# Optimization experiments

Hardware: AMD Instinct MI355X
Metric: run time of the kernel (lower is better)

Reference implementation:

```python
import jax, jax.numpy as jnp
import numpy as np

N_HEADS = 8
HEAD_DIM = 64
SCALE = HEAD_DIM ** -0.5


def setup_inputs() -> dict:
    key = jax.random.key(0)
    k1, k2, k3 = jax.random.split(key, 3)
    B, C, Hs, Ws = 8, 512, 64, 64
    x = jax.random.normal(k1, (B, C, Hs, Ws), dtype=jnp.float32)
    _h = jnp.zeros((1,), dtype=jnp.int32)  # unused arg in original forward
    # proj_in: Linear(C, 3*H*hd); stored as (in, out) so y = x @ W + b
    W_in = jax.random.normal(k2, (C, 3 * N_HEADS * HEAD_DIM), dtype=jnp.float32) * (C ** -0.5)
    b_in = jnp.zeros((3 * N_HEADS * HEAD_DIM,), dtype=jnp.float32)
    W_out = jax.random.normal(k3, (N_HEADS * HEAD_DIM, C), dtype=jnp.float32) * ((N_HEADS * HEAD_DIM) ** -0.5)
    b_out = jnp.zeros((C,), dtype=jnp.float32)
    return {"x": x, "_h": _h, "W_in": W_in, "b_in": b_in, "W_out": W_out, "b_out": b_out}


def reference(x, _h, W_in, b_in, W_out, b_out):
    in_shape = x.shape
    B, C = in_shape[0], in_shape[1]
    # (B, C, *spatial) -> (B, S, C)
    xf = x.reshape(B, C, -1).transpose(0, 2, 1)
    S = xf.shape[1]
    # fused QKV projection -> (B, S, H, 3*hd), chunk into q, k, v: (B, S, H, hd)
    qkv = (xf @ W_in + b_in).reshape(B, S, N_HEADS, 3 * HEAD_DIM)
    q, k, v = jnp.split(qkv, 3, axis=-1)
    # NOTE: faithful to the original, SDPA receives (B, S, H, hd) WITHOUT a
    # transpose to (B, H, S, hd): attention runs over the heads axis (HxH),
    # batched over (B, S).
    scores = jnp.einsum("bsqd,bskd->bsqk", q, k) * SCALE  # (B, S, H, H)
    attn = jax.nn.softmax(scores, axis=-1)
    out = jnp.einsum("bsqk,bskd->bsqd", attn, v)  # (B, S, H, hd)
    out = out.reshape(B, S, N_HEADS * HEAD_DIM)
    out = out @ W_out + b_out  # (B, S, C)
    return out.transpose(0, 2, 1).reshape(in_shape)
```

## Files before the change

### kernel.cpp

```cpp
#include <hip/hip_runtime.h>
#include <hip/hip_bf16.h>

typedef __attribute__((ext_vector_type(8))) short bh8;
typedef __attribute__((ext_vector_type(4))) float fx4;

#define GLOAD16(g, l)                                                          \
  __builtin_amdgcn_global_load_lds(                                            \
      (const __attribute__((address_space(1))) void*)(g),                      \
      (__attribute__((address_space(3))) void*)(l), 16, 0, 0)

__device__ __forceinline__ unsigned short f2bf(float f) {
  unsigned int u = __float_as_uint(f);
  u += 0x7fffu + ((u >> 16) & 1u);
  return (unsigned short)(u >> 16);
}
__device__ __forceinline__ float bf2f(short h) {
  return __uint_as_float(((unsigned int)(unsigned short)h) << 16);
}

__global__ __launch_bounds__(256) void transpose_cvt(
    const float* __restrict__ in, short* __restrict__ out, int R, int Ccols) {
  __shared__ float tile[64][65];
  const int b = blockIdx.z;
  const int c0 = blockIdx.x * 64;
  const int r0 = blockIdx.y * 64;
  const float* ip = in + (size_t)b * R * Ccols;
  short* op = out + (size_t)b * Ccols * R;
  const int tid = threadIdx.x;
  const int tx = tid & 63, ty = tid >> 6;
#pragma unroll
  for (int i = 0; i < 16; ++i) {
    int r = ty + i * 4;
    tile[tx][r] = ip[(size_t)(r0 + r) * Ccols + c0 + tx];
  }
  __syncthreads();
  const int cg = tid & 15;
  const int rr = tid >> 4;
#pragma unroll
  for (int i = 0; i < 4; ++i) {
    const int cc = i * 16 + rr;
    const unsigned int lo = (unsigned int)f2bf(tile[cc][cg * 4 + 0]) |
                            ((unsigned int)f2bf(tile[cc][cg * 4 + 1]) << 16);
    const unsigned int hi = (unsigned int)f2bf(tile[cc][cg * 4 + 2]) |
                            ((unsigned int)f2bf(tile[cc][cg * 4 + 3]) << 16);
    uint2 v; v.x = lo; v.y = hi;
    *(uint2*)&op[(size_t)(c0 + cc) * R + r0 + cg * 4] = v;
  }
}

template <int MODE, int KC>
__global__ __launch_bounds__(256) void gemm_bt(
    const short* __restrict__ A, const short* __restrict__ Bt,
    const float* __restrict__ bias, void* __restrict__ Cout,
    int M, int N, int tok0) {
  __shared__ short As[3][128 * 32] __attribute__((aligned(16)));
  __shared__ short Bs[3][128 * 32] __attribute__((aligned(16)));
  constexpr int NT = KC / 32;
  const int tid = threadIdx.x;
  const int lane = tid & 63;
  const int wv = tid >> 6;
  const int wr = wv >> 1, wc = wv & 1;

  const int nbx = gridDim.x, nby = gridDim.y;
  const int nwg = nbx * nby;
  int h = blockIdx.y * nbx + blockIdx.x;
  int L = h;
  if ((nwg & 7) == 0) {
    const int q = nwg >> 3;
    L = (h & 7) * q + (h >> 3);
  }
  int bx, by;
  if (MODE == 1) {
    by = L / nbx;
    bx = L - by * nbx;
  } else {
    bx = L / nby;
    by = L - bx * nby;
  }
  const int m0 = by * 128, n0 = bx * 128;

  const int lr = lane & 15;
  const int lk = (lane >> 4) * 8;
  const int rsw = ((lr >> 1) & 3) << 3;

  fx4 acc[4][4] = {};

  const int srow = tid >> 2;
  const int skoff = (((tid & 3) ^ ((tid >> 3) & 3)) * 8);
  const size_t abase = (size_t)(m0 + srow) * KC + skoff;
  const size_t bbase = (size_t)(n0 + srow) * KC + skoff;
  const int ldoff = wv * 1024;

  auto STAGE = [&](int kt, int slot) {
    const size_t ko = (size_t)kt * 32;
    char* lA = (char*)As[slot] + ldoff;
    char* lB = (char*)Bs[slot] + ldoff;
    GLOAD16(A + abase + ko, lA);
    GLOAD16(A + abase + (size_t)64 * KC + ko, lA + 4096);
    GLOAD16(Bt + bbase + ko, lB);
    GLOAD16(Bt + bbase + (size_t)64 * KC + ko, lB + 4096);
  };

  STAGE(0, 0);
  STAGE(1, 1);

  for (int t = 0; t < NT; ++t) {
    __builtin_amdgcn_sched_barrier(0);
    if (t < NT - 1) {
      asm volatile("s_waitcnt vmcnt(4)" ::: "memory");
    } else {
      asm volatile("s_waitcnt vmcnt(0)" ::: "memory");
    }
    __builtin_amdgcn_s_barrier();
    __builtin_amdgcn_sched_barrier(0);
    if (t + 2 < NT) STAGE(t + 2, (t + 2) % 3);
    __builtin_amdgcn_sched_barrier(0);

    const int sl = t % 3;
    bh8 af[4], bfm[4];
#pragma unroll
    for (int i = 0; i < 4; ++i) {
      af[i] = *(const bh8*)&As[sl][(wr * 64 + i * 16 + lr) * 32 + (lk ^ rsw)];
      bfm[i] = *(const bh8*)&Bs[sl][(wc * 64 + i * 16 + lr) * 32 + (lk ^ rsw)];
    }
#pragma unroll
    for (int i = 0; i < 4; ++i)
#pragma unroll
      for (int j = 0; j < 4; ++j)
        acc[i][j] = __builtin_amdgcn_mfma_f32_16x16x32_bf16(af[i], bfm[j],
                                                            acc[i][j], 0, 0, 0);
  }

  if (MODE == 1) {
    short* C = (short*)Cout;
#pragma unroll
    for (int i = 0; i < 4; ++i) {
      const int gm = m0 + wr * 64 + i * 16 + (lane >> 4) * 4;
#pragma unroll
      for (int j = 0; j < 4; ++j) {
        const int gn = n0 + wc * 64 + j * 16 + lr;
        const float bv = bias[gn];
#pragma unroll
        for (int r = 0; r < 4; ++r)
          C[(size_t)(gm + r) * N + gn] = (short)f2bf(acc[i][j][r] + bv);
      }
    }
  } else {
    float* C = (float*)Cout;
#pragma unroll
    for (int i = 0; i < 4; ++i) {
      const int ch0 = m0 + wr * 64 + i * 16 + (lane >> 4) * 4;
#pragma unroll
      for (int j = 0; j < 4; ++j) {
        const int t = tok0 + n0 + wc * 64 + j * 16 + lr;
        const int bb = t >> 12, s = t & 4095;
#pragma unroll
        for (int r = 0; r < 4; ++r) {
          const int ch = ch0 + r;
          C[((size_t)(bb * 512 + ch)) * 4096 + s] = acc[i][j][r] + bias[ch];
        }
      }
    }
  }
}

__global__ __launch_bounds__(256) void attn_kernel(
    const short* __restrict__ QKV, short* __restrict__ AO) {
  __shared__ short sq[4][1536] __attribute__((aligned(16)));
  const int tid = threadIdx.x, lane = tid & 63, wv = tid >> 6;
  const int t = blockIdx.x * 4 + wv;

  {
    const short* g = QKV + (size_t)t * 1536 + lane * 8;
    char* l = (char*)&sq[wv][0];
    GLOAD16(g, l);
    GLOAD16(g + 512, l + 1024);
    GLOAD16(g + 1024, l + 2048);
  }
  asm volatile("s_waitcnt vmcnt(0)" ::: "memory");

  const int i = lane >> 3, j = lane & 7;
  const short* q = &sq[wv][i * 192];
  const short* k = &sq[wv][j * 192 + 64];
  float s = 0.f;
#pragma unroll
  for (int c = 0; c < 8; ++c) {
    bh8 qa = *(const bh8*)&q[c * 8];
    bh8 ka = *(const bh8*)&k[c * 8];
#pragma unroll
    for (int e = 0; e < 8; ++e) s += bf2f(qa[e]) * bf2f(ka[e]);
  }
  s *= 0.125f;

  float m = s;
  m = fmaxf(m, __shfl_xor(m, 1));
  m = fmaxf(m, __shfl_xor(m, 2));
  m = fmaxf(m, __shfl_xor(m, 4));
  float p = __expf(s - m);
  float sum = p;
  sum += __shfl_xor(sum, 1);
  sum += __shfl_xor(sum, 2);
  sum += __shfl_xor(sum, 4);
  const float a = p / sum;

  float o[8] = {};
#pragma unroll
  for (int jj = 0; jj < 8; ++jj) {
    const float aj = __shfl(a, (lane & 56) | jj);
    bh8 va = *(const bh8*)&sq[wv][jj * 192 + 128 + j * 8];
#pragma unroll
    for (int e = 0; e < 8; ++e) o[e] += aj * bf2f(va[e]);
  }
  bh8 ov;
#pragma unroll
  for (int e = 0; e < 8; ++e) ov[e] = (short)f2bf(o[e]);
  *(bh8*)&AO[(size_t)t * 512 + i * 64 + j * 8] = ov;
}

extern "C" void kernel_launch(void* const* d_in, const int* in_sizes, int n_in,
                              void* d_out, int out_size, void* d_ws,
                              size_t ws_size, hipStream_t stream) {
  const float* x = (const float*)d_in[0];
  const float* W_in = (const float*)d_in[2];
  const float* b_in = (const float*)d_in[3];
  const float* W_out = (const float*)d_in[4];
  const float* b_out = (const float*)d_in[5];
  float* out = (float*)d_out;

  short* Xbf = (short*)d_ws;
  short* WinT = Xbf + (size_t)32768 * 512;
  short* WoutT = WinT + (size_t)1536 * 512;
  short* QKVc = WoutT + (size_t)512 * 512;

  const size_t fixed_bytes =
      ((size_t)32768 * 512 + (size_t)1536 * 512 + (size_t)512 * 512) * 2;
  int NC = 1;
  while (NC < 256 &&
         fixed_bytes + ((size_t)32768 / NC) * 1536 * 2 > ws_size)
    NC <<= 1;
  const int Mc = 32768 / NC;

  transpose_cvt<<<dim3(64, 8, 8), 256, 0, stream>>>(x, Xbf, 512, 4096);
  transpose_cvt<<<dim3(24, 8, 1), 256, 0, stream>>>(W_in, WinT, 512, 1536);
  transpose_cvt<<<dim3(8, 8, 1), 256, 0, stream>>>(W_out, WoutT, 512, 512);

  for (int c = 0; c < NC; ++c) {
    const int t0 = c * Mc;
    short* Ach = Xbf + (size_t)t0 * 512;
    gemm_bt<1, 512><<<dim3(12, Mc / 128), 256, 0, stream>>>(Ach, WinT, b_in,
                                                            QKVc, Mc, 1536, 0);
    attn_kernel<<<dim3(Mc / 4), 256, 0, stream>>>(QKVc, Ach);
    gemm_bt<2, 512><<<dim3(Mc / 128, 4), 256, 0, stream>>>(WoutT, Ach, b_out,
                                                           out, 512, Mc, t0);
  }
}
```

Baseline: 243.7 us.

## Enlarge GEMM tiles to 256x256 with 8 waves and split-stage double buffering

The bf16 GEMM kernel moves from 128x128 tiles with 4 waves and a 3-slot LDS ring to 256x256 tiles with 8 waves (2x4 wave grid, 128x64 per wave) and a double buffer. Each k-step is split into two halves: the loads for one operand are issued first and the loads for the other are issued mid-step, with s_setprio raised around the MFMA bursts. The goal is more data reuse per global load and better overlap of loads with compute. In exchange it uses more accumulator registers and launches fewer, larger blocks, which could lower occupancy or leave some CUs idle on the small grids.

```diff
diff --git a/kernel.cpp b/kernel.cpp
--- a/kernel.cpp
+++ b/kernel.cpp
@@ -49,17 +49,18 @@
 }
 
 template <int MODE, int KC>
-__global__ __launch_bounds__(256) void gemm_bt(
+__global__ __launch_bounds__(512, 2) void gemm_bt(
     const short* __restrict__ A, const short* __restrict__ Bt,
     const float* __restrict__ bias, void* __restrict__ Cout,
     int M, int N, int tok0) {
-  __shared__ short As[3][128 * 32] __attribute__((aligned(16)));
-  __shared__ short Bs[3][128 * 32] __attribute__((aligned(16)));
+  __shared__ short As[2][8192] __attribute__((aligned(16)));
+  __shared__ short Bs[2][8192] __attribute__((aligned(16)));
   constexpr int NT = KC / 32;
   const int tid = threadIdx.x;
   const int lane = tid & 63;
   const int wv = tid >> 6;
-  const int wr = wv >> 1, wc = wv & 1;
+  const int wm = wv >> 2;
+  const int wn = wv & 3;
 
   const int nbx = gridDim.x, nby = gridDim.y;
   const int nwg = nbx * nby;
@@ -69,76 +70,106 @@
     const int q = nwg >> 3;
     L = (h & 7) * q + (h >> 3);
   }
-  int bx, by;
-  if (MODE == 1) {
-    by = L / nbx;
-    bx = L - by * nbx;
-  } else {
-    bx = L / nby;
-    by = L - bx * nby;
-  }
-  const int m0 = by * 128, n0 = bx * 128;
+  const int bx = L / nby;
+  const int by = L - bx * nby;
+  const int m0 = by * 256, n0 = bx * 256;
 
   const int lr = lane & 15;
-  const int lk = (lane >> 4) * 8;
-  const int rsw = ((lr >> 1) & 3) << 3;
-
-  fx4 acc[4][4] = {};
+  const int kg = lane >> 4;
+  const int rsw = (kg ^ ((lr >> 1) & 3)) * 8;
 
   const int srow = tid >> 2;
-  const int skoff = (((tid & 3) ^ ((tid >> 3) & 3)) * 8);
-  const size_t abase = (size_t)(m0 + srow) * KC + skoff;
-  const size_t bbase = (size_t)(n0 + srow) * KC + skoff;
-  const int ldoff = wv * 1024;
-
-  auto STAGE = [&](int kt, int slot) {
-    const size_t ko = (size_t)kt * 32;
-    char* lA = (char*)As[slot] + ldoff;
-    char* lB = (char*)Bs[slot] + ldoff;
-    GLOAD16(A + abase + ko, lA);
-    GLOAD16(A + abase + (size_t)64 * KC + ko, lA + 4096);
-    GLOAD16(Bt + bbase + ko, lB);
-    GLOAD16(Bt + bbase + (size_t)64 * KC + ko, lB + 4096);
-  };
-
-  STAGE(0, 0);
-  STAGE(1, 1);
-
-  for (int t = 0; t < NT; ++t) {
+  const int schunk = ((tid & 3) ^ ((tid >> 3) & 3)) * 8;
+  const size_t abase = (size_t)(m0 + srow) * KC + schunk;
+  const size_t bbase = (size_t)(n0 + srow) * KC + schunk;
+  const int doff = tid * 16;
+
+#define SA(kt, b, hh)                                                          \
+  GLOAD16(A + abase + (size_t)(hh)*128 * KC + (kt)*32,                         \
+          (char*)&As[b][0] + (hh)*8192 + doff)
+#define SB(kt, b, hh)                                                          \
+  GLOAD16(Bt + bbase + (size_t)(hh)*128 * KC + (kt)*32,                        \
+          (char*)&Bs[b][0] + (hh)*8192 + doff)
+
+  fx4 acc[8][4] = {};
+
+  SA(0, 0, 0); SA(0, 0, 1); SB(0, 0, 0); SB(0, 0, 1);
+
+#define MF16(a0_, a1_, a2_, a3_, r0_)                                          \
+  {                                                                            \
+    _Pragma("unroll") for (int j = 0; j < 4; ++j) {                            \
+      acc[r0_ + 0][j] =                                                        \
+          __builtin_amdgcn_mfma_f32_16x16x32_bf16(a0_, bb[j], acc[r0_ + 0][j], 0, 0, 0); \
+      acc[r0_ + 1][j] =                                                        \
+          __builtin_amdgcn_mfma_f32_16x16x32_bf16(a1_, bb[j], acc[r0_ + 1][j], 0, 0, 0); \
+      acc[r0_ + 2][j] =                                                        \
+          __builtin_amdgcn_mfma_f32_16x16x32_bf16(a2_, bb[j], acc[r0_ + 2][j], 0, 0, 0); \
+      acc[r0_ + 3][j] =                                                        \
+          __builtin_amdgcn_mfma_f32_16x16x32_bf16(a3_, bb[j], acc[r0_ + 3][j], 0, 0, 0); \
+    }                                                                          \
+  }
+
+  for (int g = 0; g < NT; ++g) {
+    const int buf = g & 1, nb = buf ^ 1;
+    const short* Ab = &As[buf][0];
+    const short* Bb = &Bs[buf][0];
+
     __builtin_amdgcn_sched_barrier(0);
-    if (t < NT - 1) {
-      asm volatile("s_waitcnt vmcnt(4)" ::: "memory");
+    if (g + 1 < NT) {
+      if (MODE == 1) { SA(g + 1, nb, 0); SA(g + 1, nb, 1); }
+      else           { SB(g + 1, nb, 0); SB(g + 1, nb, 1); }
+      __builtin_amdgcn_sched_barrier(0);
+      asm volatile("s_waitcnt vmcnt(2)" ::: "memory");
     } else {
       asm volatile("s_waitcnt vmcnt(0)" ::: "memory");
     }
     __builtin_amdgcn_s_barrier();
     __builtin_amdgcn_sched_barrier(0);
-    if (t + 2 < NT) STAGE(t + 2, (t + 2) % 3);
-    __builtin_amdgcn_sched_barrier(0);
-
-    const int sl = t % 3;
-    bh8 af[4], bfm[4];
-#pragma unroll
-    for (int i = 0; i < 4; ++i) {
-      af[i] = *(const bh8*)&As[sl][(wr * 64 + i * 16 + lr) * 32 + (lk ^ rsw)];
-      bfm[i] = *(const bh8*)&Bs[sl][(wc * 64 + i * 16 + lr) * 32 + (lk ^ rsw)];
-    }
-#pragma unroll
-    for (int i = 0; i < 4; ++i)
+    {
+      bh8 a0 = *(const bh8*)&Ab[(wm * 128 + 0 + lr) * 32 + rsw];
+      bh8 a1 = *(const bh8*)&Ab[(wm * 128 + 16 + lr) * 32 + rsw];
+      bh8 a2 = *(const bh8*)&Ab[(wm * 128 + 32 + lr) * 32 + rsw];
+      bh8 a3 = *(const bh8*)&Ab[(wm * 128 + 48 + lr) * 32 + rsw];
+      bh8 bb[4];
 #pragma unroll
       for (int j = 0; j < 4; ++j)
-        acc[i][j] = __builtin_amdgcn_mfma_f32_16x16x32_bf16(af[i], bfm[j],
-                                                            acc[i][j], 0, 0, 0);
+        bb[j] = *(const bh8*)&Bb[(wn * 64 + j * 16 + lr) * 32 + rsw];
+      asm volatile("s_waitcnt lgkmcnt(0)" ::: "memory");
+      __builtin_amdgcn_sched_barrier(0);
+      __builtin_amdgcn_s_setprio(1);
+      MF16(a0, a1, a2, a3, 0);
+      __builtin_amdgcn_s_setprio(0);
+      __builtin_amdgcn_sched_barrier(0);
+      __builtin_amdgcn_s_barrier();
+
+      a0 = *(const bh8*)&Ab[(wm * 128 + 64 + 0 + lr) * 32 + rsw];
+      a1 = *(const bh8*)&Ab[(wm * 128 + 64 + 16 + lr) * 32 + rsw];
+      a2 = *(const bh8*)&Ab[(wm * 128 + 64 + 32 + lr) * 32 + rsw];
+      a3 = *(const bh8*)&Ab[(wm * 128 + 64 + 48 + lr) * 32 + rsw];
+      if (g + 1 < NT) {
+        if (MODE == 1) { SB(g + 1, nb, 0); SB(g + 1, nb, 1); }
+        else           { SA(g + 1, nb, 0); SA(g + 1, nb, 1); }
+      }
+      __builtin_amdgcn_sched_barrier(0);
+      __builtin_amdgcn_s_barrier();
+      asm volatile("s_waitcnt lgkmcnt(0)" ::: "memory");
+      __builtin_amdgcn_sched_barrier(0);
+      __builtin_amdgcn_s_setprio(1);
+      MF16(a0, a1, a2, a3, 4);
+      __builtin_amdgcn_s_setprio(0);
+      __builtin_amdgcn_sched_barrier(0);
+      __builtin_amdgcn_s_barrier();
+    }
   }
 
   if (MODE == 1) {
     short* C = (short*)Cout;
 #pragma unroll
-    for (int i = 0; i < 4; ++i) {
-      const int gm = m0 + wr * 64 + i * 16 + (lane >> 4) * 4;
+    for (int i = 0; i < 8; ++i) {
+      const int gm = m0 + wm * 128 + i * 16 + kg * 4;
 #pragma unroll
       for (int j = 0; j < 4; ++j) {
-        const int gn = n0 + wc * 64 + j * 16 + lr;
+        const int gn = n0 + wn * 64 + j * 16 + lr;
         const float bv = bias[gn];
 #pragma unroll
         for (int r = 0; r < 4; ++r)
@@ -148,20 +179,23 @@
   } else {
     float* C = (float*)Cout;
 #pragma unroll
-    for (int i = 0; i < 4; ++i) {
-      const int ch0 = m0 + wr * 64 + i * 16 + (lane >> 4) * 4;
+    for (int i = 0; i < 8; ++i) {
+      const int ch0 = m0 + wm * 128 + i * 16 + kg * 4;
 #pragma unroll
       for (int j = 0; j < 4; ++j) {
-        const int t = tok0 + n0 + wc * 64 + j * 16 + lr;
-        const int bb = t >> 12, s = t & 4095;
+        const int t = tok0 + n0 + wn * 64 + j * 16 + lr;
+        const int bb2 = t >> 12, s = t & 4095;
 #pragma unroll
         for (int r = 0; r < 4; ++r) {
           const int ch = ch0 + r;
-          C[((size_t)(bb * 512 + ch)) * 4096 + s] = acc[i][j][r] + bias[ch];
+          C[((size_t)(bb2 * 512 + ch)) * 4096 + s] = acc[i][j][r] + bias[ch];
         }
       }
     }
   }
+#undef SA
+#undef SB
+#undef MF16
 }
 
 __global__ __launch_bounds__(256) void attn_kernel(
@@ -235,7 +269,7 @@
   const size_t fixed_bytes =
       ((size_t)32768 * 512 + (size_t)1536 * 512 + (size_t)512 * 512) * 2;
   int NC = 1;
-  while (NC < 256 &&
+  while (NC < 128 &&
          fixed_bytes + ((size_t)32768 / NC) * 1536 * 2 > ws_size)
     NC <<= 1;
   const int Mc = 32768 / NC;
@@ -247,10 +281,10 @@
   for (int c = 0; c < NC; ++c) {
     const int t0 = c * Mc;
     short* Ach = Xbf + (size_t)t0 * 512;
-    gemm_bt<1, 512><<<dim3(12, Mc / 128), 256, 0, stream>>>(Ach, WinT, b_in,
-                                                            QKVc, Mc, 1536, 0);
+    gemm_bt<1, 512><<<dim3(6, Mc / 256), 512, 0, stream>>>(Ach, WinT, b_in,
+                                                           QKVc, Mc, 1536, 0);
     attn_kernel<<<dim3(Mc / 4), 256, 0, stream>>>(QKVc, Ach);
-    gemm_bt<2, 512><<<dim3(Mc / 128, 4), 256, 0, stream>>>(WoutT, Ach, b_out,
+    gemm_bt<2, 512><<<dim3(Mc / 256, 2), 512, 0, stream>>>(WoutT, Ach, b_out,
                                                            out, 512, Mc, t0);
   }
 }
```

Result: slower. 258.4 us (+6.0%).

## Enlarge GEMM tiles to 256x128 with 8 waves and 64-wide K stages

Applied to the files above, without the earlier changes.

Both GEMMs now use 512-thread blocks computing 256x128 output tiles with K staged in 64-element chunks. A is triple-buffered and B double-buffered, with a new 8-chunk XOR swizzle in LDS. The goal is to reuse each B tile across twice as many rows and to halve the number of barriers per K. In exchange each block uses more LDS (about 128 KB) and occupancy drops to one block per CU, and the grids get smaller. The chunk-count cap is also lowered.

```diff
diff --git a/kernel.cpp b/kernel.cpp
--- a/kernel.cpp
+++ b/kernel.cpp
@@ -49,17 +49,18 @@
 }
 
 template <int MODE, int KC>
-__global__ __launch_bounds__(256) void gemm_bt(
+__global__ __launch_bounds__(512, 1) void gemm_bt(
     const short* __restrict__ A, const short* __restrict__ Bt,
     const float* __restrict__ bias, void* __restrict__ Cout,
     int M, int N, int tok0) {
-  __shared__ short As[3][128 * 32] __attribute__((aligned(16)));
-  __shared__ short Bs[3][128 * 32] __attribute__((aligned(16)));
-  constexpr int NT = KC / 32;
+  __shared__ short As[3][256 * 64] __attribute__((aligned(16)));
+  __shared__ short Bs[2][128 * 64] __attribute__((aligned(16)));
+  constexpr int NS = KC / 64;
   const int tid = threadIdx.x;
   const int lane = tid & 63;
   const int wv = tid >> 6;
-  const int wr = wv >> 1, wc = wv & 1;
+  const int wm = wv >> 1;
+  const int wn = wv & 1;
 
   const int nbx = gridDim.x, nby = gridDim.y;
   const int nwg = nbx * nby;
@@ -77,68 +78,80 @@
     bx = L / nby;
     by = L - bx * nby;
   }
-  const int m0 = by * 128, n0 = bx * 128;
+  const int m0 = by * 256, n0 = bx * 128;
 
   const int lr = lane & 15;
-  const int lk = (lane >> 4) * 8;
-  const int rsw = ((lr >> 1) & 3) << 3;
+  const int kg = lane >> 4;
+
+  const int schunk = ((tid & 7) ^ ((tid >> 3) & 7)) * 8;
+  const size_t abase = (size_t)(m0 + (tid >> 3)) * KC + schunk;
+  const size_t bbase = (size_t)(n0 + (tid >> 3)) * KC + schunk;
+
+  auto STAGE_A = [&](int s) {
+    const int buf = s % 3;
+    const size_t ko = (size_t)s * 64;
+#pragma unroll
+    for (int q = 0; q < 4; ++q)
+      GLOAD16(A + abase + (size_t)q * 64 * KC + ko,
+              (char*)&As[buf][0] + q * 8192 + tid * 16);
+  };
+  auto STAGE_B = [&](int s) {
+    const int buf = s & 1;
+    const size_t ko = (size_t)s * 64;
+#pragma unroll
+    for (int q = 0; q < 2; ++q)
+      GLOAD16(Bt + bbase + (size_t)q * 64 * KC + ko,
+              (char*)&Bs[buf][0] + q * 8192 + tid * 16);
+  };
 
   fx4 acc[4][4] = {};
 
-  const int srow = tid >> 2;
-  const int skoff = (((tid & 3) ^ ((tid >> 3) & 3)) * 8);
-  const size_t abase = (size_t)(m0 + srow) * KC + skoff;
-  const size_t bbase = (size_t)(n0 + srow) * KC + skoff;
-  const int ldoff = wv * 1024;
-
-  auto STAGE = [&](int kt, int slot) {
-    const size_t ko = (size_t)kt * 32;
-    char* lA = (char*)As[slot] + ldoff;
-    char* lB = (char*)Bs[slot] + ldoff;
-    GLOAD16(A + abase + ko, lA);
-    GLOAD16(A + abase + (size_t)64 * KC + ko, lA + 4096);
-    GLOAD16(Bt + bbase + ko, lB);
-    GLOAD16(Bt + bbase + (size_t)64 * KC + ko, lB + 4096);
-  };
-
-  STAGE(0, 0);
-  STAGE(1, 1);
-
-  for (int t = 0; t < NT; ++t) {
+  STAGE_B(0);
+  STAGE_A(0);
+  STAGE_A(1);
+
+  for (int s = 0; s < NS; ++s) {
     __builtin_amdgcn_sched_barrier(0);
-    if (t < NT - 1) {
+    if (s < NS - 1) {
       asm volatile("s_waitcnt vmcnt(4)" ::: "memory");
     } else {
       asm volatile("s_waitcnt vmcnt(0)" ::: "memory");
     }
     __builtin_amdgcn_s_barrier();
     __builtin_amdgcn_sched_barrier(0);
-    if (t + 2 < NT) STAGE(t + 2, (t + 2) % 3);
+    if (s + 1 < NS) STAGE_B(s + 1);
+    if (s + 2 < NS) STAGE_A(s + 2);
     __builtin_amdgcn_sched_barrier(0);
 
-    const int sl = t % 3;
-    bh8 af[4], bfm[4];
-#pragma unroll
-    for (int i = 0; i < 4; ++i) {
-      af[i] = *(const bh8*)&As[sl][(wr * 64 + i * 16 + lr) * 32 + (lk ^ rsw)];
-      bfm[i] = *(const bh8*)&Bs[sl][(wc * 64 + i * 16 + lr) * 32 + (lk ^ rsw)];
-    }
-#pragma unroll
-    for (int i = 0; i < 4; ++i)
+    const short* Ab = &As[s % 3][0];
+    const short* Bb = &Bs[s & 1][0];
+#pragma unroll
+    for (int kk = 0; kk < 2; ++kk) {
+      const int cs = ((kk * 4 + kg) ^ (lr & 7)) * 8;
+      bh8 af[4], bf[4];
+#pragma unroll
+      for (int i = 0; i < 4; ++i)
+        af[i] = *(const bh8*)&Ab[(wm * 64 + i * 16 + lr) * 64 + cs];
 #pragma unroll
       for (int j = 0; j < 4; ++j)
-        acc[i][j] = __builtin_amdgcn_mfma_f32_16x16x32_bf16(af[i], bfm[j],
-                                                            acc[i][j], 0, 0, 0);
+        bf[j] = *(const bh8*)&Bb[(wn * 64 + j * 16 + lr) * 64 + cs];
+#pragma unroll
+      for (int i = 0; i < 4; ++i)
+#pragma unroll
+        for (int j = 0; j < 4; ++j)
+          acc[i][j] = __builtin_amdgcn_mfma_f32_16x16x32_bf16(
+              af[i], bf[j], acc[i][j], 0, 0, 0);
+    }
   }
 
   if (MODE == 1) {
     short* C = (short*)Cout;
 #pragma unroll
     for (int i = 0; i < 4; ++i) {
-      const int gm = m0 + wr * 64 + i * 16 + (lane >> 4) * 4;
+      const int gm = m0 + wm * 64 + i * 16 + kg * 4;
 #pragma unroll
       for (int j = 0; j < 4; ++j) {
-        const int gn = n0 + wc * 64 + j * 16 + lr;
+        const int gn = n0 + wn * 64 + j * 16 + lr;
         const float bv = bias[gn];
 #pragma unroll
         for (int r = 0; r < 4; ++r)
@@ -149,15 +162,15 @@
     float* C = (float*)Cout;
 #pragma unroll
     for (int i = 0; i < 4; ++i) {
-      const int ch0 = m0 + wr * 64 + i * 16 + (lane >> 4) * 4;
+      const int ch0 = m0 + wm * 64 + i * 16 + kg * 4;
 #pragma unroll
       for (int j = 0; j < 4; ++j) {
-        const int t = tok0 + n0 + wc * 64 + j * 16 + lr;
-        const int bb = t >> 12, s = t & 4095;
+        const int t = tok0 + n0 + wn * 64 + j * 16 + lr;
+        const int bb2 = t >> 12, sp = t & 4095;
 #pragma unroll
         for (int r = 0; r < 4; ++r) {
           const int ch = ch0 + r;
-          C[((size_t)(bb * 512 + ch)) * 4096 + s] = acc[i][j][r] + bias[ch];
+          C[((size_t)(bb2 * 512 + ch)) * 4096 + sp] = acc[i][j][r] + bias[ch];
         }
       }
     }
@@ -235,7 +248,7 @@
   const size_t fixed_bytes =
       ((size_t)32768 * 512 + (size_t)1536 * 512 + (size_t)512 * 512) * 2;
   int NC = 1;
-  while (NC < 256 &&
+  while (NC < 64 &&
          fixed_bytes + ((size_t)32768 / NC) * 1536 * 2 > ws_size)
     NC <<= 1;
   const int Mc = 32768 / NC;
@@ -247,10 +260,10 @@
   for (int c = 0; c < NC; ++c) {
     const int t0 = c * Mc;
     short* Ach = Xbf + (size_t)t0 * 512;
-    gemm_bt<1, 512><<<dim3(12, Mc / 128), 256, 0, stream>>>(Ach, WinT, b_in,
+    gemm_bt<1, 512><<<dim3(12, Mc / 256), 512, 0, stream>>>(Ach, WinT, b_in,
                                                             QKVc, Mc, 1536, 0);
     attn_kernel<<<dim3(Mc / 4), 256, 0, stream>>>(QKVc, Ach);
-    gemm_bt<2, 512><<<dim3(Mc / 128, 4), 256, 0, stream>>>(WoutT, Ach, b_out,
+    gemm_bt<2, 512><<<dim3(Mc / 128, 2), 512, 0, stream>>>(WoutT, Ach, b_out,
                                                            out, 512, Mc, t0);
   }
 }
```

Measured after the change: 256.3 us. +5.2%, slower.
